# Kernel optimization log

Hardware: AMD Instinct MI355X
Metric: run time of the kernel (lower is better)

The kernel has to match this reference:

```python
import jax, jax.numpy as jnp
import numpy as np

NU, NN, NS = 50000, 20000, 2000
D_IN, D_HID, D_OUT = 128, 128, 64
LRELU_SLOPE = 0.01  # torch F.leaky_relu default


def _edges(k, n_src, n_dst, e):
    k1, k2 = jax.random.split(k)
    return (jax.random.randint(k1, (e,), 0, n_src, dtype=jnp.int32),
            jax.random.randint(k2, (e,), 0, n_dst, dtype=jnp.int32))


def setup_inputs() -> dict:
    key = jax.random.key(0)
    ks = jax.random.split(key, 32)
    fs, fd = _edges(ks[0], NU, NU, 500000)
    ps, pd = _edges(ks[1], NU, NN, 300000)
    pbs, pbd = _edges(ks[2], NN, NU, 300000)
    us, ud = _edges(ks[3], NS, NN, 150000)
    ubs, ubd = _edges(ks[4], NN, NS, 150000)
    s = 0.05
    inp = {
        "x_user": jax.random.normal(ks[5], (NU, D_IN), jnp.float32),
        "x_news": jax.random.normal(ks[6], (NN, D_IN), jnp.float32),
        "x_source": jax.random.normal(ks[7], (NS, D_IN), jnp.float32),
        # stacked per-relation GraphConv params, order:
        # [follows, posts, posted_by, publishes, published_by]
        "W1": jax.random.normal(ks[8], (5, D_IN, D_HID), jnp.float32) * s,
        "b1": jnp.zeros((5, D_HID), jnp.float32),
        "W2": jax.random.normal(ks[9], (5, D_HID, D_HID), jnp.float32) * s,
        "b2": jnp.zeros((5, D_HID), jnp.float32),
        "Wu": jax.random.normal(ks[10], (D_HID, D_OUT), jnp.float32) * s,
        "bu": jnp.zeros((D_OUT,), jnp.float32),
        "Wn": jax.random.normal(ks[11], (D_HID, D_OUT), jnp.float32) * s,
        "bn": jnp.zeros((D_OUT,), jnp.float32),
        "Ws": jax.random.normal(ks[12], (D_HID, D_OUT), jnp.float32) * s,
        "bs": jnp.zeros((D_OUT,), jnp.float32),
        "follows_src": fs, "follows_dst": fd,
        "posts_src": ps, "posts_dst": pd,
        "postedby_src": pbs, "postedby_dst": pbd,
        "publishes_src": us, "publishes_dst": ud,
        "publishedby_src": ubs, "publishedby_dst": ubd,
    }
    return inp


def _gconv(x_src, src, dst, n_dst, W, b):
    """DGL GraphConv, norm='both': D_dst^-1/2 A D_src^-1/2 X W + b."""
    n_src = x_src.shape[0]
    ones = jnp.ones(src.shape[0], x_src.dtype)
    dout = jnp.clip(jax.ops.segment_sum(ones, src, num_segments=n_src), 1.0)
    din = jnp.clip(jax.ops.segment_sum(ones, dst, num_segments=n_dst), 1.0)
    h = (x_src * jax.lax.rsqrt(dout)[:, None]) @ W  # transform before gather
    agg = jax.ops.segment_sum(h[src], dst, num_segments=n_dst)
    return agg * jax.lax.rsqrt(din)[:, None] + b


def _hetero_layer(xu, xn, xs, E, W, b):
    # mean aggregation across relations sharing a dst type
    hu = 0.5 * (_gconv(xu, E["fs"], E["fd"], NU, W[0], b[0])
                + _gconv(xn, E["pbs"], E["pbd"], NU, W[2], b[2]))
    hn = 0.5 * (_gconv(xu, E["ps"], E["pd"], NN, W[1], b[1])
                + _gconv(xs, E["us"], E["ud"], NN, W[3], b[3]))
    hs = _gconv(xn, E["ubs"], E["ubd"], NS, W[4], b[4])
    return hu, hn, hs


def reference(x_user, x_news, x_source, W1, b1, W2, b2, Wu, bu, Wn, bn, Ws, bs,
              follows_src, follows_dst, posts_src, posts_dst,
              postedby_src, postedby_dst, publishes_src, publishes_dst,
              publishedby_src, publishedby_dst):
    E = {"fs": follows_src, "fd": follows_dst, "ps": posts_src, "pd": posts_dst,
         "pbs": postedby_src, "pbd": postedby_dst, "us": publishes_src,
         "ud": publishes_dst, "ubs": publishedby_src, "ubd": publishedby_dst}
    lrelu = lambda v: jax.nn.leaky_relu(v, LRELU_SLOPE)
    hu, hn, hs = _hetero_layer(x_user, x_news, x_source, E, W1, b1)
    hu, hn, hs = lrelu(hu), lrelu(hn), lrelu(hs)
    hu, hn, hs = _hetero_layer(hu, hn, hs, E, W2, b2)
    hu, hn, hs = lrelu(hu), lrelu(hn), lrelu(hs)
    ou = hu @ Wu + bu
    on = hn @ Wn + bn
    os_ = hs @ Ws + bs
    return (ou, on, os_, hu, hn, hs)
```

## Files before the change

kernel.cpp:

```cpp
#include <hip/hip_runtime.h>

#define LRELU 0.01f

static const int kNU = 50000, kNN = 20000, kNS = 2000;
static const int DOUT_OFF[5] = {0, 100000, 170000, 240000, 262000};
static const int DIN_OFF[5]  = {50000, 150000, 190000, 242000, 282000};
static const int RP_OFF[5]   = {0, 50001, 70002, 120003, 140004};
static const int CSR_OFF[5]  = {0, 500000, 800000, 1100000, 1250000};

using bf16x8 = __attribute__((ext_vector_type(8))) short;
using u16x8  = __attribute__((ext_vector_type(8))) unsigned short;
using f32x4  = __attribute__((ext_vector_type(4))) float;

__device__ __forceinline__ float bf2f(unsigned short u) {
  return __uint_as_float(((unsigned)u) << 16);
}
__device__ __forceinline__ unsigned short f2bf(float f) {
  unsigned u = __float_as_uint(f);
  u += 0x7FFFu + ((u >> 16) & 1u);
  return (unsigned short)(u >> 16);
}


struct TJob { const float* X; const float* W; unsigned short* Y; int M; };
struct PrepJob { const float* W0; const float* W128; unsigned short* hi;
                 unsigned short* lo; int NOUT; int lgK; int bstart; };
struct AArgs { const int* esrc[5]; const int* edst[5]; int* pos; int* partial;
               TJob tj[5]; PrepJob pj[6]; };

__device__ __forceinline__ void transform_body(const TJob& p, int bxl, int t) {
  int w = t >> 6, l = t & 63;
  int lo16 = l & 15, hi4 = l >> 4;
  int m0 = bxl * 64;
  int M = p.M;
  f32x4 acc[4][2] = {};
  for (int s = 0; s < 4; ++s) {
    int kbase = s * 32 + hi4 * 8;
    bf16x8 af[4];
#pragma unroll
    for (int mf = 0; mf < 4; ++mf) {
      int row = m0 + mf * 16 + lo16;
      row = row < M ? row : M - 1;
      const float* xr = &p.X[(size_t)row * 128 + kbase];
      float4 xa = *(const float4*)xr;
      float4 xb = *(const float4*)(xr + 4);
      af[mf][0] = (short)f2bf(xa.x); af[mf][1] = (short)f2bf(xa.y);
      af[mf][2] = (short)f2bf(xa.z); af[mf][3] = (short)f2bf(xa.w);
      af[mf][4] = (short)f2bf(xb.x); af[mf][5] = (short)f2bf(xb.y);
      af[mf][6] = (short)f2bf(xb.z); af[mf][7] = (short)f2bf(xb.w);
    }
#pragma unroll
    for (int nf = 0; nf < 2; ++nf) {
      int n = (w * 2 + nf) * 16 + lo16;
      bf16x8 bh, bl;
#pragma unroll
      for (int j = 0; j < 8; ++j) {
        float wv = p.W[(size_t)(kbase + j) * 128 + n];
        unsigned short h = f2bf(wv);
        bh[j] = (short)h;
        bl[j] = (short)f2bf(wv - bf2f(h));
      }
#pragma unroll
      for (int mf = 0; mf < 4; ++mf) {
        acc[mf][nf] = __builtin_amdgcn_mfma_f32_16x16x32_bf16(af[mf], bh, acc[mf][nf], 0, 0, 0);
        acc[mf][nf] = __builtin_amdgcn_mfma_f32_16x16x32_bf16(af[mf], bl, acc[mf][nf], 0, 0, 0);
      }
    }
  }
#pragma unroll
  for (int nf = 0; nf < 2; ++nf) {
    int col = (w * 2 + nf) * 16 + lo16;
#pragma unroll
    for (int mf = 0; mf < 4; ++mf) {
#pragma unroll
      for (int rr = 0; rr < 4; ++rr) {
        int row = m0 + mf * 16 + hi4 * 4 + rr;
        if (row < M) p.Y[(size_t)row * 128 + col] = f2bf(acc[mf][nf][rr]);
      }
    }
  }
}

__global__ __launch_bounds__(256) void k_histA(AArgs a) {
  __shared__ int hbin[8192];
  int bx = blockIdx.x;
  int t = threadIdx.x;
  if (bx < 336) {
    constexpr int DSTART[6] = {0, 112, 160, 272, 320, 336};
    constexpr int NDT[5] = {50000, 20000, 50000, 20000, 2000};
    constexpr int CS[5]  = {31250, 18750, 18750, 9375, 9375};
    constexpr int EE[5]  = {500000, 300000, 300000, 150000, 150000};
    constexpr int PB[5]  = {0, 800000, 1120000, 1920000, 2240000};
    constexpr int COFF[5] = {0, 500000, 800000, 1100000, 1250000};
    int r = 0;
    while (bx >= DSTART[r + 1]) ++r;
    int local = bx - DSTART[r];
    int g = local >> 4, c = local & 15;
    int nd = NDT[r];
    int gbase = g * 8192;
    int gend = gbase + 8192 < nd ? gbase + 8192 : nd;
    const int* dst = a.edst[r];
    int* pos = a.pos + COFF[r];
    int elo = c * CS[r];
    int ehi = elo + CS[r] < EE[r] ? elo + CS[r] : EE[r];
    for (int j = t; j < 8192; j += 256) hbin[j] = 0;
    __syncthreads();
    for (int e = elo + t; e < ehi; e += 256) {
      int d = dst[e];
      if (d >= gbase && d < gend) pos[e] = atomicAdd(&hbin[d - gbase], 1);
    }
    __syncthreads();
    int* out = a.partial + PB[r] + (size_t)c * nd + gbase;
    int nn = gend - gbase;
    for (int j = t; j < nn; j += 256) out[j] = hbin[j];
  } else if (bx < 672) {
    constexpr int OSTART[6] = {0, 112, 224, 272, 288, 336};
    constexpr int NST[5] = {50000, 50000, 20000, 2000, 20000};
    constexpr int CS[5]  = {31250, 18750, 18750, 9375, 9375};
    constexpr int EE[5]  = {500000, 300000, 300000, 150000, 150000};
    constexpr int PB[5]  = {2272000, 3072000, 3872000, 4192000, 4224000};
    int idx = bx - 336;
    int r = 0;
    while (idx >= OSTART[r + 1]) ++r;
    int local = idx - OSTART[r];
    int g = local >> 4, c = local & 15;
    int ns = NST[r];
    int gbase = g * 8192;
    int gend = gbase + 8192 < ns ? gbase + 8192 : ns;
    const int* src = a.esrc[r];
    int elo = c * CS[r];
    int ehi = elo + CS[r] < EE[r] ? elo + CS[r] : EE[r];
    for (int j = t; j < 8192; j += 256) hbin[j] = 0;
    __syncthreads();
    for (int e = elo + t; e < ehi; e += 256) {
      int s = src[e];
      if (s >= gbase && s < gend) atomicAdd(&hbin[s - gbase], 1);
    }
    __syncthreads();
    int* out = a.partial + PB[r] + (size_t)c * ns + gbase;
    int nn = gend - gbase;
    for (int j = t; j < nn; j += 256) out[j] = hbin[j];
  } else if (bx < 2894) {
    constexpr int TSTART[6] = {0, 782, 1564, 1877, 1909, 2222};
    int ti = bx - 672, r = 0;
    while (ti >= TSTART[r + 1]) ++r;
    transform_body(a.tj[r], ti - TSTART[r], t);
  } else {
    int b = bx - 2894, ji = 0;
    while (ji < 5 && b >= a.pj[ji + 1].bstart) ++ji;
    PrepJob p = a.pj[ji];
    int eidx = (b - p.bstart) * 256 + t;
    int K = 1 << p.lgK;
    int n = eidx >> p.lgK, k = eidx & (K - 1);
    if (n >= p.NOUT) return;
    float w = (k < 128) ? p.W0[k * p.NOUT + n] : p.W128[(k - 128) * p.NOUT + n];
    unsigned short h = f2bf(w);
    float res = w - bf2f(h);
    p.hi[n * K + k] = h;
    p.lo[n * K + k] = f2bf(res);
  }
}


struct BArgs { int* partial; int* cnt; float* rs; };

__global__ __launch_bounds__(256) void k_scanB(BArgs a) {
  int bx = blockIdx.x;
  int t = threadIdx.x;
  if (bx < 555) {
    int i = bx * 256 + t;
    if (i >= 142000) return;
    constexpr int NDT[5] = {50000, 20000, 50000, 20000, 2000};
    constexpr int PB[5]  = {0, 800000, 1120000, 1920000, 2240000};
    constexpr int DOFF[5] = {50000, 150000, 190000, 242000, 282000};
    int r, d;
    if      (i < 50000)  { r = 0; d = i; }
    else if (i < 70000)  { r = 1; d = i - 50000; }
    else if (i < 120000) { r = 2; d = i - 70000; }
    else if (i < 140000) { r = 3; d = i - 120000; }
    else                 { r = 4; d = i - 140000; }
    int nd = NDT[r];
    int* p = a.partial + PB[r] + d;
    int run = 0;
#pragma unroll
    for (int c = 0; c < 16; ++c) {
      int v = p[(size_t)c * nd];
      p[(size_t)c * nd] = run;
      run += v;
    }
    a.cnt[DOFF[r] + d] = run;
    a.rs[DOFF[r] + d] = rsqrtf((float)(run > 1 ? run : 1));
  } else {
    int i = (bx - 555) * 256 + t;
    if (i >= 142000) return;
    constexpr int NST[5] = {50000, 50000, 20000, 2000, 20000};
    constexpr int PB[5]  = {2272000, 3072000, 3872000, 4192000, 4224000};
    constexpr int OOFF[5] = {0, 100000, 170000, 240000, 262000};
    int r, s;
    if      (i < 50000)  { r = 0; s = i; }
    else if (i < 100000) { r = 1; s = i - 50000; }
    else if (i < 120000) { r = 2; s = i - 100000; }
    else if (i < 122000) { r = 3; s = i - 120000; }
    else                 { r = 4; s = i - 122000; }
    int ns = NST[r];
    const int* p = a.partial + PB[r] + s;
    int sum = 0;
#pragma unroll
    for (int c = 0; c < 16; ++c) sum += p[(size_t)c * ns];
    a.rs[OOFF[r] + s] = rsqrtf((float)(sum > 1 ? sum : 1));
  }
}


struct S3Args { const int* cnt; int* rp; };

__global__ __launch_bounds__(256) void k_scan3(S3Args a) {
  constexpr int CSTART[6] = {0, 49, 69, 118, 138, 140};
  constexpr int NDT[5] = {50000, 20000, 50000, 20000, 2000};
  constexpr int DOFF[5] = {50000, 150000, 190000, 242000, 282000};
  constexpr int RPOFF[5] = {0, 50001, 70002, 120003, 140004};
  int bx = blockIdx.x, r = 0;
  while (bx >= CSTART[r + 1]) ++r;
  int chunk = bx - CSTART[r];
  int nch = CSTART[r + 1] - CSTART[r];
  int n = NDT[r];
  const int* cnt = a.cnt + DOFF[r];
  int* rp = a.rp + RPOFF[r];
  int t = threadIdx.x;
  __shared__ int sd[256];
  __shared__ int choff_sh;
  int lim = chunk * 1024;
  int pre = 0;
  for (int j = t; j < lim; j += 256) pre += cnt[j];
  sd[t] = pre;
  __syncthreads();
  for (int off = 128; off > 0; off >>= 1) {
    if (t < off) sd[t] += sd[t + off];
    __syncthreads();
  }
  if (t == 0) choff_sh = sd[0];
  __syncthreads();
  int idx0 = lim + t * 4;
  int v[4];
#pragma unroll
  for (int j = 0; j < 4; ++j) v[j] = (idx0 + j < n) ? cnt[idx0 + j] : 0;
  int tsum = v[0] + v[1] + v[2] + v[3];
  sd[t] = tsum;
  __syncthreads();
  for (int s = 1; s < 256; s <<= 1) {
    int add = (t >= s) ? sd[t - s] : 0;
    __syncthreads();
    sd[t] += add;
    __syncthreads();
  }
  int off = choff_sh + sd[t] - tsum;
#pragma unroll
  for (int j = 0; j < 4; ++j) {
    if (idx0 + j < n) rp[idx0 + j] = off;
    off += v[j];
  }
  if (chunk == nch - 1 && t == 255) rp[n] = choff_sh + sd[255];
}


struct CArgs { const int* esrc[5]; const int* edst[5]; const int* pos;
               const int* rp; const int* partial; int* csr; };

__global__ __launch_bounds__(256) void k_buildC(CArgs a) {
  constexpr int ESTART[6] = {0, 1954, 3126, 4298, 4884, 5470};
  constexpr int NDT[5] = {50000, 20000, 50000, 20000, 2000};
  constexpr int CS[5]  = {31250, 18750, 18750, 9375, 9375};
  constexpr int EE[5]  = {500000, 300000, 300000, 150000, 150000};
  constexpr int PB[5]  = {0, 800000, 1120000, 1920000, 2240000};
  constexpr int RPOFF[5] = {0, 50001, 70002, 120003, 140004};
  constexpr int COFF[5] = {0, 500000, 800000, 1100000, 1250000};
  int bx = blockIdx.x, r = 0;
  while (bx >= ESTART[r + 1]) ++r;
  int i = (bx - ESTART[r]) * 256 + threadIdx.x;
  if (i < EE[r]) {
    int d = a.edst[r][i];
    int c = i / CS[r];
    int slot = a.rp[RPOFF[r] + d] + a.partial[PB[r] + (size_t)c * NDT[r] + d]
             + a.pos[COFF[r] + i];
    a.csr[COFF[r] + slot] = a.esrc[r][i];
  }
}


#define GROW(vv, cc)                                                              \
  _Pragma("unroll") for (int q = 0; q < 8; ++q)                                   \
      acc[q] = fmaf(__uint_as_float(((unsigned)(unsigned short)vv[q]) << 16), cc, acc[q]);

__device__ __forceinline__ void gat_accum(const int* __restrict__ rp,
    const int* __restrict__ csr, const unsigned short* __restrict__ Y,
    const float* __restrict__ rso, int wid, int sub, float* acc) {
  int e0 = rp[wid], e1 = rp[wid + 1];
  for (int base = e0; base < e1; base += 16) {
    int m = e1 - base;
    if (m > 16) m = 16;
    int ei = base + (sub < m ? sub : 0);
    int se = csr[ei];
    float sc = rso[se];
    if (m == 16) {
      bf16x8 v[16];
#pragma unroll
      for (int j = 0; j < 16; ++j) {
        int sj = __shfl(se, j, 16);
        v[j] = *(const bf16x8*)&Y[(size_t)sj * 128 + sub * 8];
      }
#pragma unroll
      for (int j = 0; j < 16; ++j) {
        float cj = __shfl(sc, j, 16);
        GROW(v[j], cj)
      }
    } else {
      int j = 0;
      for (; j + 8 <= m; j += 8) {
        int s0 = __shfl(se, j, 16), s1 = __shfl(se, j + 1, 16);
        int s2 = __shfl(se, j + 2, 16), s3 = __shfl(se, j + 3, 16);
        int s4 = __shfl(se, j + 4, 16), s5 = __shfl(se, j + 5, 16);
        int s6 = __shfl(se, j + 6, 16), s7 = __shfl(se, j + 7, 16);
        float c0 = __shfl(sc, j, 16), c1 = __shfl(sc, j + 1, 16);
        float c2 = __shfl(sc, j + 2, 16), c3 = __shfl(sc, j + 3, 16);
        float c4 = __shfl(sc, j + 4, 16), c5 = __shfl(sc, j + 5, 16);
        float c6 = __shfl(sc, j + 6, 16), c7 = __shfl(sc, j + 7, 16);
        bf16x8 v0 = *(const bf16x8*)&Y[(size_t)s0 * 128 + sub * 8];
        bf16x8 v1 = *(const bf16x8*)&Y[(size_t)s1 * 128 + sub * 8];
        bf16x8 v2 = *(const bf16x8*)&Y[(size_t)s2 * 128 + sub * 8];
        bf16x8 v3 = *(const bf16x8*)&Y[(size_t)s3 * 128 + sub * 8];
        bf16x8 v4 = *(const bf16x8*)&Y[(size_t)s4 * 128 + sub * 8];
        bf16x8 v5 = *(const bf16x8*)&Y[(size_t)s5 * 128 + sub * 8];
        bf16x8 v6 = *(const bf16x8*)&Y[(size_t)s6 * 128 + sub * 8];
        bf16x8 v7 = *(const bf16x8*)&Y[(size_t)s7 * 128 + sub * 8];
        GROW(v0, c0) GROW(v1, c1) GROW(v2, c2) GROW(v3, c3)
        GROW(v4, c4) GROW(v5, c5) GROW(v6, c6) GROW(v7, c7)
      }
      for (; j < m; ++j) {
        int s0 = __shfl(se, j, 16);
        float c0 = __shfl(sc, j, 16);
        bf16x8 v0 = *(const bf16x8*)&Y[(size_t)s0 * 128 + sub * 8];
        GROW(v0, c0)
      }
    }
  }
}


struct G1Rel { const int* rp; const int* csr; const unsigned short* Y;
               const float* rso; const float* rsi; };
struct G1Args { G1Rel rel[5]; const float* b;
                unsigned short* hU; unsigned short* hN; unsigned short* hS; };

__global__ __launch_bounds__(256) void k_gather1(G1Args a) {
  int bx = blockIdx.x;
  int t = threadIdx.x;
  int sub = t & 15;
  float acc[8], tot[8];
#pragma unroll
  for (int q = 0; q < 8; ++q) acc[q] = 0.f;
  if (bx < 3125) {
    int wid = bx * 16 + (t >> 4);
    gat_accum(a.rel[0].rp, a.rel[0].csr, a.rel[0].Y, a.rel[0].rso, wid, sub, acc);
    float s0 = a.rel[0].rsi[wid];
#pragma unroll
    for (int q = 0; q < 8; ++q) { tot[q] = s0 * acc[q]; acc[q] = 0.f; }
    gat_accum(a.rel[2].rp, a.rel[2].csr, a.rel[2].Y, a.rel[2].rso, wid, sub, acc);
    float s2 = a.rel[2].rsi[wid];
    const float* b0 = a.b;
    const float* b2 = a.b + 2 * 128;
    u16x8 o;
#pragma unroll
    for (int q = 0; q < 8; ++q) {
      float v = 0.5f * (tot[q] + s2 * acc[q] + b0[sub * 8 + q] + b2[sub * 8 + q]);
      v = v >= 0.f ? v : LRELU * v;
      o[q] = f2bf(v);
    }
    *(u16x8*)&a.hU[(size_t)wid * 128 + sub * 8] = o;
  } else if (bx < 4375) {
    int wid = (bx - 3125) * 16 + (t >> 4);
    gat_accum(a.rel[1].rp, a.rel[1].csr, a.rel[1].Y, a.rel[1].rso, wid, sub, acc);
    float s1 = a.rel[1].rsi[wid];
#pragma unroll
    for (int q = 0; q < 8; ++q) { tot[q] = s1 * acc[q]; acc[q] = 0.f; }
    gat_accum(a.rel[3].rp, a.rel[3].csr, a.rel[3].Y, a.rel[3].rso, wid, sub, acc);
    float s3 = a.rel[3].rsi[wid];
    const float* b1v = a.b + 128;
    const float* b3 = a.b + 3 * 128;
    u16x8 o;
#pragma unroll
    for (int q = 0; q < 8; ++q) {
      float v = 0.5f * (tot[q] + s3 * acc[q] + b1v[sub * 8 + q] + b3[sub * 8 + q]);
      v = v >= 0.f ? v : LRELU * v;
      o[q] = f2bf(v);
    }
    *(u16x8*)&a.hN[(size_t)wid * 128 + sub * 8] = o;
  } else {
    int wid = (bx - 4375) * 16 + (t >> 4);
    gat_accum(a.rel[4].rp, a.rel[4].csr, a.rel[4].Y, a.rel[4].rso, wid, sub, acc);
    float s4 = a.rel[4].rsi[wid];
    const float* b4 = a.b + 4 * 128;
    u16x8 o;
#pragma unroll
    for (int q = 0; q < 8; ++q) {
      float v = s4 * acc[q] + b4[sub * 8 + q];
      v = v >= 0.f ? v : LRELU * v;
      o[q] = f2bf(v);
    }
    *(u16x8*)&a.hS[(size_t)wid * 128 + sub * 8] = o;
  }
}


struct RelG {
  const int* rp; const int* csr; const unsigned short* xb;
  const float* rso; const float* rsi;
  unsigned short* out; int stride; int ooff; int nd;
};
struct GArgs { RelG rel[5]; };

__global__ __launch_bounds__(256) void k_gather(GArgs a) {
  constexpr int GSTART[6] = {0, 3125, 4375, 7500, 8750, 8875};
  int bx = blockIdx.x, r = 0;
  while (bx >= GSTART[r + 1]) ++r;
  RelG g = a.rel[r];
  int t = threadIdx.x;
  int sub = t & 15;
  int wid = (bx - GSTART[r]) * 16 + (t >> 4);
  if (wid >= g.nd) return;
  float acc[8];
#pragma unroll
  for (int q = 0; q < 8; ++q) acc[q] = 0.f;
  gat_accum(g.rp, g.csr, g.xb, g.rso, wid, sub, acc);
  float si = g.rsi[wid];
  u16x8 o;
#pragma unroll
  for (int q = 0; q < 8; ++q) o[q] = f2bf(acc[q] * si);
  *(u16x8*)&g.out[(size_t)wid * g.stride + g.ooff + sub * 8] = o;
}


struct MJob { const unsigned short* A; const unsigned short* Wh; const unsigned short* Wl;
              const float* b0; const float* b1; float scale; int lrelu;
              float* H; int ldh; unsigned short* Hb; int M; int bstart; };
struct MArgs { MJob j[3]; };

template <int KCH, int NW>
__device__ __forceinline__ void mgemm_body(const MJob& p, int bxl) {
  constexpr int KP = KCH * 128;
  int t = threadIdx.x;
  int w = t >> 6, l = t & 63;
  int lo16 = l & 15, hi4 = l >> 4;
  int m0 = bxl * 64;
  int M = p.M;
  const unsigned short* A = p.A;
  f32x4 acc[4][NW] = {};
  for (int s = 0; s < KP / 32; ++s) {
    int kbase = s * 32 + hi4 * 8;
    bf16x8 af[4];
#pragma unroll
    for (int mf = 0; mf < 4; ++mf) {
      int row = m0 + mf * 16 + lo16;
      row = row < M ? row : M - 1;
      af[mf] = *(const bf16x8*)&A[(size_t)row * KP + kbase];
    }
#pragma unroll
    for (int nf = 0; nf < NW; ++nf) {
      int n = (w * NW + nf) * 16 + lo16;
      bf16x8 bh = *(const bf16x8*)&p.Wh[(size_t)n * KP + kbase];
      bf16x8 bl = *(const bf16x8*)&p.Wl[(size_t)n * KP + kbase];
#pragma unroll
      for (int mf = 0; mf < 4; ++mf) {
        acc[mf][nf] = __builtin_amdgcn_mfma_f32_16x16x32_bf16(af[mf], bh, acc[mf][nf], 0, 0, 0);
        acc[mf][nf] = __builtin_amdgcn_mfma_f32_16x16x32_bf16(af[mf], bl, acc[mf][nf], 0, 0, 0);
      }
    }
  }
#pragma unroll
  for (int nf = 0; nf < NW; ++nf) {
    int col = (w * NW + nf) * 16 + lo16;
    float bs = p.b0[col];
    if (p.b1) bs += p.b1[col];
#pragma unroll
    for (int mf = 0; mf < 4; ++mf) {
#pragma unroll
      for (int rr = 0; rr < 4; ++rr) {
        int row = m0 + mf * 16 + hi4 * 4 + rr;
        if (row < M) {
          float o = p.scale * (acc[mf][nf][rr] + bs);
          if (p.lrelu) o = o >= 0.f ? o : LRELU * o;
          if (p.H) p.H[(size_t)row * p.ldh + col] = o;
          if (p.Hb) p.Hb[(size_t)row * p.ldh + col] = f2bf(o);
        }
      }
    }
  }
}

__global__ __launch_bounds__(256) void k_mgemm3(MArgs a) {
  int bx = blockIdx.x;
  if (bx < a.j[1].bstart)      mgemm_body<2, 2>(a.j[0], bx);
  else if (bx < a.j[2].bstart) mgemm_body<2, 2>(a.j[1], bx - a.j[1].bstart);
  else                         mgemm_body<1, 2>(a.j[2], bx - a.j[2].bstart);
}

__global__ __launch_bounds__(256) void k_proj3(MArgs a) {
  int bx = blockIdx.x;
  if (bx < a.j[1].bstart)      mgemm_body<1, 1>(a.j[0], bx);
  else if (bx < a.j[2].bstart) mgemm_body<1, 1>(a.j[1], bx - a.j[1].bstart);
  else                         mgemm_body<1, 1>(a.j[2], bx - a.j[2].bstart);
}


extern "C" void kernel_launch(void* const* d_in, const int* in_sizes, int n_in,
                              void* d_out, int out_size, void* d_ws, size_t ws_size,
                              hipStream_t stream) {
  const float* xu = (const float*)d_in[0];
  const float* xn = (const float*)d_in[1];
  const float* xs = (const float*)d_in[2];
  const float* W1 = (const float*)d_in[3];
  const float* b1 = (const float*)d_in[4];
  const float* W2 = (const float*)d_in[5];
  const float* b2 = (const float*)d_in[6];
  const float* Wu = (const float*)d_in[7];
  const float* bu = (const float*)d_in[8];
  const float* Wn = (const float*)d_in[9];
  const float* bn = (const float*)d_in[10];
  const float* Wsrc = (const float*)d_in[11];
  const float* bsrc = (const float*)d_in[12];
  const int* SRC[5] = {(const int*)d_in[13], (const int*)d_in[15], (const int*)d_in[17],
                       (const int*)d_in[19], (const int*)d_in[21]};
  const int* DST[5] = {(const int*)d_in[14], (const int*)d_in[16], (const int*)d_in[18],
                       (const int*)d_in[20], (const int*)d_in[22]};

  int* ws_i = (int*)d_ws;
  int* rp = ws_i;
  int* csr = ws_i + 142008;
  int* pos = ws_i + 1542008;
  int* cnt = ws_i + 2942328;
  float* rs = (float*)(ws_i + 3226328);
  unsigned short* wt = (unsigned short*)(rs + 284000);
  unsigned short* aggU = wt + 376832;
  unsigned short* aggN = aggU + 12800000;
  unsigned short* aggS = aggN + 5120000;
  unsigned short* xbU = aggS + 256000;
  unsigned short* xbN = xbU + 6400000;
  unsigned short* xbS = xbN + 2560000;

  unsigned short* L2U_h = wt + 163840, * L2U_l = wt + 196608;
  unsigned short* L2N_h = wt + 229376, * L2N_l = wt + 262144;
  unsigned short* L2S_h = wt + 294912, * L2S_l = wt + 311296;
  unsigned short* PU_h = wt + 327680, * PU_l = wt + 335872;
  unsigned short* PN_h = wt + 344064, * PN_l = wt + 352256;
  unsigned short* PS_h = wt + 360448, * PS_l = wt + 368640;

  float* outf = (float*)d_out;
  float* ou = outf;
  float* on = outf + 3200000;
  float* osrc = outf + 4480000;
  float* hu = outf + 4608000;
  float* hn = outf + 11008000;
  float* hs = outf + 13568000;

  int* partial = (int*)outf;

  unsigned short* Yb = (unsigned short*)(outf + 4608000);
  unsigned short* Y0 = Yb;
  unsigned short* Y1 = Y0 + 6400000;
  unsigned short* Y2 = Y1 + 6400000;
  unsigned short* Y3 = Y2 + 2560000;
  unsigned short* Y4 = Y3 + 256000;

  AArgs aa;
  for (int r = 0; r < 5; ++r) { aa.esrc[r] = SRC[r]; aa.edst[r] = DST[r]; }
  aa.pos = pos;
  aa.partial = partial;
  aa.tj[0] = {xu, W1 + 0 * 16384, Y0, kNU};
  aa.tj[1] = {xu, W1 + 1 * 16384, Y1, kNU};
  aa.tj[2] = {xn, W1 + 2 * 16384, Y2, kNN};
  aa.tj[3] = {xs, W1 + 3 * 16384, Y3, kNS};
  aa.tj[4] = {xn, W1 + 4 * 16384, Y4, kNN};
  aa.pj[0] = {W2, W2 + 2 * 16384, L2U_h, L2U_l, 128, 8, 0};
  aa.pj[1] = {W2 + 16384, W2 + 3 * 16384, L2N_h, L2N_l, 128, 8, 128};
  aa.pj[2] = {W2 + 4 * 16384, nullptr, L2S_h, L2S_l, 128, 7, 256};
  aa.pj[3] = {Wu, nullptr, PU_h, PU_l, 64, 7, 320};
  aa.pj[4] = {Wn, nullptr, PN_h, PN_l, 64, 7, 352};
  aa.pj[5] = {Wsrc, nullptr, PS_h, PS_l, 64, 7, 384};
  k_histA<<<3310, 256, 0, stream>>>(aa);

  BArgs ba = {partial, cnt, rs};
  k_scanB<<<1110, 256, 0, stream>>>(ba);

  S3Args s3 = {cnt, rp};
  k_scan3<<<140, 256, 0, stream>>>(s3);

  CArgs ca;
  for (int r = 0; r < 5; ++r) { ca.esrc[r] = SRC[r]; ca.edst[r] = DST[r]; }
  ca.pos = pos;
  ca.rp = rp;
  ca.partial = partial;
  ca.csr = csr;
  k_buildC<<<5470, 256, 0, stream>>>(ca);

  G1Args g1;
  const unsigned short* YT[5] = {Y0, Y1, Y2, Y3, Y4};
  for (int r = 0; r < 5; ++r)
    g1.rel[r] = {rp + RP_OFF[r], csr + CSR_OFF[r], YT[r],
                 rs + DOUT_OFF[r], rs + DIN_OFF[r]};
  g1.b = b1;
  g1.hU = xbU; g1.hN = xbN; g1.hS = xbS;
  k_gather1<<<4500, 256, 0, stream>>>(g1);

  {
    const unsigned short* XIN[5] = {xbU, xbU, xbN, xbS, xbN};
    unsigned short* OUT[5] = {aggU, aggN, aggU, aggN, aggS};
    const int OSTR[5] = {256, 256, 256, 256, 128};
    const int OOFF[5] = {0, 0, 128, 128, 0};
    GArgs ga;
    for (int r = 0; r < 5; ++r)
      ga.rel[r] = {rp + RP_OFF[r], csr + CSR_OFF[r], XIN[r], rs + DOUT_OFF[r],
                   rs + DIN_OFF[r], OUT[r], OSTR[r], OOFF[r],
                   (r == 0 || r == 2) ? kNU : (r == 4 ? kNS : kNN)};
    k_gather<<<8875, 256, 0, stream>>>(ga);
    MArgs ma;
    ma.j[0] = {aggU, L2U_h, L2U_l, b2, b2 + 2 * 128, 0.5f, 1, hu, 128, xbU, kNU, 0};
    ma.j[1] = {aggN, L2N_h, L2N_l, b2 + 128, b2 + 3 * 128, 0.5f, 1, hn, 128, xbN, kNN, 782};
    ma.j[2] = {aggS, L2S_h, L2S_l, b2 + 4 * 128, nullptr, 1.0f, 1, hs, 128, xbS, kNS, 1095};
    k_mgemm3<<<1127, 256, 0, stream>>>(ma);
  }

  MArgs pm;
  pm.j[0] = {xbU, PU_h, PU_l, bu, nullptr, 1.0f, 0, ou, 64, nullptr, kNU, 0};
  pm.j[1] = {xbN, PN_h, PN_l, bn, nullptr, 1.0f, 0, on, 64, nullptr, kNN, 782};
  pm.j[2] = {xbS, PS_h, PS_l, bsrc, nullptr, 1.0f, 0, osrc, 64, nullptr, kNS, 1095};
  k_proj3<<<1127, 256, 0, stream>>>(pm);
}
```

Measured before the change: 330.5 us.

## Transform-before-gather for layer 2 and pack histogram bins as 16-bit pairs

Layer 2 used to gather first and then run a concatenated-K GEMM. It now applies the per-relation weight transform first (k_trans5) and then gathers through a fused kernel that does the combine, bias, leaky-relu and both fp32 and bf16 stores, matching how layer 1 is done. This swaps the wide 256-col aggregate buffers for per-relation transformed features, so the larger gather now reads 128-col bf16 rows of transformed features per edge and the GEMM shrinks to K=128. The histogram kernel also packs two 16-bit counters per shared int, so each block covers 16384 bins and fewer blocks are launched. This relies on no bin count exceeding 65535 per chunk and on the in-place writes to xb buffers being ordered safely.

```diff
diff --git a/kernel.cpp b/kernel.cpp
--- a/kernel.cpp
+++ b/kernel.cpp
@@ -23,10 +23,10 @@
 
 
 struct TJob { const float* X; const float* W; unsigned short* Y; int M; };
-struct PrepJob { const float* W0; const float* W128; unsigned short* hi;
-                 unsigned short* lo; int NOUT; int lgK; int bstart; };
+struct PrepJob { const float* W0; unsigned short* hi; unsigned short* lo;
+                 int NOUT; int bstart; };
 struct AArgs { const int* esrc[5]; const int* edst[5]; int* pos; int* partial;
-               TJob tj[5]; PrepJob pj[6]; };
+               TJob tj[5]; PrepJob pj[8]; };
 
 __device__ __forceinline__ void transform_body(const TJob& p, int bxl, int t) {
   int w = t >> 6, l = t & 63;
@@ -82,11 +82,11 @@
 }
 
 __global__ __launch_bounds__(256) void k_histA(AArgs a) {
-  __shared__ int hbin[8192];
+  __shared__ unsigned hbin[8192];
   int bx = blockIdx.x;
   int t = threadIdx.x;
-  if (bx < 336) {
-    constexpr int DSTART[6] = {0, 112, 160, 272, 320, 336};
+  if (bx < 208) {
+    constexpr int DSTART[6] = {0, 64, 96, 160, 192, 208};
     constexpr int NDT[5] = {50000, 20000, 50000, 20000, 2000};
     constexpr int CS[5]  = {31250, 18750, 18750, 9375, 9375};
     constexpr int EE[5]  = {500000, 300000, 300000, 150000, 150000};
@@ -97,8 +97,8 @@
     int local = bx - DSTART[r];
     int g = local >> 4, c = local & 15;
     int nd = NDT[r];
-    int gbase = g * 8192;
-    int gend = gbase + 8192 < nd ? gbase + 8192 : nd;
+    int gbase = g * 16384;
+    int gend = gbase + 16384 < nd ? gbase + 16384 : nd;
     const int* dst = a.edst[r];
     int* pos = a.pos + COFF[r];
     int elo = c * CS[r];
@@ -107,26 +107,32 @@
     __syncthreads();
     for (int e = elo + t; e < ehi; e += 256) {
       int d = dst[e];
-      if (d >= gbase && d < gend) pos[e] = atomicAdd(&hbin[d - gbase], 1);
+      if (d >= gbase && d < gend) {
+        int bin = d - gbase;
+        int sh = (bin & 1) * 16;
+        unsigned old = atomicAdd(&hbin[bin >> 1], 1u << sh);
+        pos[e] = (int)((old >> sh) & 0xffffu);
+      }
     }
     __syncthreads();
     int* out = a.partial + PB[r] + (size_t)c * nd + gbase;
     int nn = gend - gbase;
-    for (int j = t; j < nn; j += 256) out[j] = hbin[j];
-  } else if (bx < 672) {
-    constexpr int OSTART[6] = {0, 112, 224, 272, 288, 336};
+    for (int j = t; j < nn; j += 256)
+      out[j] = (int)((hbin[j >> 1] >> ((j & 1) * 16)) & 0xffffu);
+  } else if (bx < 416) {
+    constexpr int OSTART[6] = {0, 64, 128, 160, 176, 208};
     constexpr int NST[5] = {50000, 50000, 20000, 2000, 20000};
     constexpr int CS[5]  = {31250, 18750, 18750, 9375, 9375};
     constexpr int EE[5]  = {500000, 300000, 300000, 150000, 150000};
     constexpr int PB[5]  = {2272000, 3072000, 3872000, 4192000, 4224000};
-    int idx = bx - 336;
+    int idx = bx - 208;
     int r = 0;
     while (idx >= OSTART[r + 1]) ++r;
     int local = idx - OSTART[r];
     int g = local >> 4, c = local & 15;
     int ns = NST[r];
-    int gbase = g * 8192;
-    int gend = gbase + 8192 < ns ? gbase + 8192 : ns;
+    int gbase = g * 16384;
+    int gend = gbase + 16384 < ns ? gbase + 16384 : ns;
     const int* src = a.esrc[r];
     int elo = c * CS[r];
     int ehi = elo + CS[r] < EE[r] ? elo + CS[r] : EE[r];
@@ -134,30 +140,31 @@
     __syncthreads();
     for (int e = elo + t; e < ehi; e += 256) {
       int s = src[e];
-      if (s >= gbase && s < gend) atomicAdd(&hbin[s - gbase], 1);
+      if (s >= gbase && s < gend)
+        atomicAdd(&hbin[(s - gbase) >> 1], 1u << (((s - gbase) & 1) * 16));
     }
     __syncthreads();
     int* out = a.partial + PB[r] + (size_t)c * ns + gbase;
     int nn = gend - gbase;
-    for (int j = t; j < nn; j += 256) out[j] = hbin[j];
-  } else if (bx < 2894) {
+    for (int j = t; j < nn; j += 256)
+      out[j] = (int)((hbin[j >> 1] >> ((j & 1) * 16)) & 0xffffu);
+  } else if (bx < 2638) {
     constexpr int TSTART[6] = {0, 782, 1564, 1877, 1909, 2222};
-    int ti = bx - 672, r = 0;
+    int ti = bx - 416, r = 0;
     while (ti >= TSTART[r + 1]) ++r;
     transform_body(a.tj[r], ti - TSTART[r], t);
   } else {
-    int b = bx - 2894, ji = 0;
-    while (ji < 5 && b >= a.pj[ji + 1].bstart) ++ji;
+    int b = bx - 2638, ji = 0;
+    while (ji < 7 && b >= a.pj[ji + 1].bstart) ++ji;
     PrepJob p = a.pj[ji];
     int eidx = (b - p.bstart) * 256 + t;
-    int K = 1 << p.lgK;
-    int n = eidx >> p.lgK, k = eidx & (K - 1);
+    int n = eidx >> 7, k = eidx & 127;
     if (n >= p.NOUT) return;
-    float w = (k < 128) ? p.W0[k * p.NOUT + n] : p.W128[(k - 128) * p.NOUT + n];
+    float w = p.W0[k * p.NOUT + n];
     unsigned short h = f2bf(w);
     float res = w - bf2f(h);
-    p.hi[n * K + k] = h;
-    p.lo[n * K + k] = f2bf(res);
+    p.hi[n * 128 + k] = h;
+    p.lo[n * 128 + k] = f2bf(res);
   }
 }
 
@@ -411,38 +418,9 @@
 }
 
 
-struct RelG {
-  const int* rp; const int* csr; const unsigned short* xb;
-  const float* rso; const float* rsi;
-  unsigned short* out; int stride; int ooff; int nd;
-};
-struct GArgs { RelG rel[5]; };
-
-__global__ __launch_bounds__(256) void k_gather(GArgs a) {
-  constexpr int GSTART[6] = {0, 3125, 4375, 7500, 8750, 8875};
-  int bx = blockIdx.x, r = 0;
-  while (bx >= GSTART[r + 1]) ++r;
-  RelG g = a.rel[r];
-  int t = threadIdx.x;
-  int sub = t & 15;
-  int wid = (bx - GSTART[r]) * 16 + (t >> 4);
-  if (wid >= g.nd) return;
-  float acc[8];
-#pragma unroll
-  for (int q = 0; q < 8; ++q) acc[q] = 0.f;
-  gat_accum(g.rp, g.csr, g.xb, g.rso, wid, sub, acc);
-  float si = g.rsi[wid];
-  u16x8 o;
-#pragma unroll
-  for (int q = 0; q < 8; ++q) o[q] = f2bf(acc[q] * si);
-  *(u16x8*)&g.out[(size_t)wid * g.stride + g.ooff + sub * 8] = o;
-}
-
-
 struct MJob { const unsigned short* A; const unsigned short* Wh; const unsigned short* Wl;
               const float* b0; const float* b1; float scale; int lrelu;
               float* H; int ldh; unsigned short* Hb; int M; int bstart; };
-struct MArgs { MJob j[3]; };
 
 template <int KCH, int NW>
 __device__ __forceinline__ void mgemm_body(const MJob& p, int bxl) {
@@ -478,7 +456,7 @@
 #pragma unroll
   for (int nf = 0; nf < NW; ++nf) {
     int col = (w * NW + nf) * 16 + lo16;
-    float bs = p.b0[col];
+    float bs = p.b0 ? p.b0[col] : 0.f;
     if (p.b1) bs += p.b1[col];
 #pragma unroll
     for (int mf = 0; mf < 4; ++mf) {
@@ -496,18 +474,90 @@
   }
 }
 
-__global__ __launch_bounds__(256) void k_mgemm3(MArgs a) {
+struct M5Args { MJob j[5]; };
+__global__ __launch_bounds__(256) void k_trans5(M5Args a) {
   int bx = blockIdx.x;
-  if (bx < a.j[1].bstart)      mgemm_body<2, 2>(a.j[0], bx);
-  else if (bx < a.j[2].bstart) mgemm_body<2, 2>(a.j[1], bx - a.j[1].bstart);
-  else                         mgemm_body<1, 2>(a.j[2], bx - a.j[2].bstart);
-}
-
+  int ji = 0;
+  while (ji < 4 && bx >= a.j[ji + 1].bstart) ++ji;
+  mgemm_body<1, 2>(a.j[ji], bx - a.j[ji].bstart);
+}
+
+struct MArgs { MJob j[3]; };
 __global__ __launch_bounds__(256) void k_proj3(MArgs a) {
   int bx = blockIdx.x;
   if (bx < a.j[1].bstart)      mgemm_body<1, 1>(a.j[0], bx);
   else if (bx < a.j[2].bstart) mgemm_body<1, 1>(a.j[1], bx - a.j[1].bstart);
   else                         mgemm_body<1, 1>(a.j[2], bx - a.j[2].bstart);
+}
+
+
+struct G2Args { G1Rel rel[5]; const float* b;
+                float* HU; float* HN; float* HS;
+                unsigned short* hU; unsigned short* hN; unsigned short* hS; };
+
+__device__ __forceinline__ void g2_store(float* H, unsigned short* Hb,
+                                         int wid, int sub, const float* v) {
+  float4 f0 = {v[0], v[1], v[2], v[3]};
+  float4 f1 = {v[4], v[5], v[6], v[7]};
+  *(float4*)&H[(size_t)wid * 128 + sub * 8] = f0;
+  *(float4*)&H[(size_t)wid * 128 + sub * 8 + 4] = f1;
+  u16x8 o;
+#pragma unroll
+  for (int q = 0; q < 8; ++q) o[q] = f2bf(v[q]);
+  *(u16x8*)&Hb[(size_t)wid * 128 + sub * 8] = o;
+}
+
+__global__ __launch_bounds__(256) void k_gather2(G2Args a) {
+  int bx = blockIdx.x;
+  int t = threadIdx.x;
+  int sub = t & 15;
+  float acc[8], tot[8], v[8];
+#pragma unroll
+  for (int q = 0; q < 8; ++q) acc[q] = 0.f;
+  if (bx < 3125) {
+    int wid = bx * 16 + (t >> 4);
+    gat_accum(a.rel[0].rp, a.rel[0].csr, a.rel[0].Y, a.rel[0].rso, wid, sub, acc);
+    float s0 = a.rel[0].rsi[wid];
+#pragma unroll
+    for (int q = 0; q < 8; ++q) { tot[q] = s0 * acc[q]; acc[q] = 0.f; }
+    gat_accum(a.rel[2].rp, a.rel[2].csr, a.rel[2].Y, a.rel[2].rso, wid, sub, acc);
+    float s2 = a.rel[2].rsi[wid];
+    const float* b0 = a.b;
+    const float* b2 = a.b + 2 * 128;
+#pragma unroll
+    for (int q = 0; q < 8; ++q) {
+      float x = 0.5f * (tot[q] + s2 * acc[q] + b0[sub * 8 + q] + b2[sub * 8 + q]);
+      v[q] = x >= 0.f ? x : LRELU * x;
+    }
+    g2_store(a.HU, a.hU, wid, sub, v);
+  } else if (bx < 4375) {
+    int wid = (bx - 3125) * 16 + (t >> 4);
+    gat_accum(a.rel[1].rp, a.rel[1].csr, a.rel[1].Y, a.rel[1].rso, wid, sub, acc);
+    float s1 = a.rel[1].rsi[wid];
+#pragma unroll
+    for (int q = 0; q < 8; ++q) { tot[q] = s1 * acc[q]; acc[q] = 0.f; }
+    gat_accum(a.rel[3].rp, a.rel[3].csr, a.rel[3].Y, a.rel[3].rso, wid, sub, acc);
+    float s3 = a.rel[3].rsi[wid];
+    const float* b1v = a.b + 128;
+    const float* b3 = a.b + 3 * 128;
+#pragma unroll
+    for (int q = 0; q < 8; ++q) {
+      float x = 0.5f * (tot[q] + s3 * acc[q] + b1v[sub * 8 + q] + b3[sub * 8 + q]);
+      v[q] = x >= 0.f ? x : LRELU * x;
+    }
+    g2_store(a.HN, a.hN, wid, sub, v);
+  } else {
+    int wid = (bx - 4375) * 16 + (t >> 4);
+    gat_accum(a.rel[4].rp, a.rel[4].csr, a.rel[4].Y, a.rel[4].rso, wid, sub, acc);
+    float s4 = a.rel[4].rsi[wid];
+    const float* b4 = a.b + 4 * 128;
+#pragma unroll
+    for (int q = 0; q < 8; ++q) {
+      float x = s4 * acc[q] + b4[sub * 8 + q];
+      v[q] = x >= 0.f ? x : LRELU * x;
+    }
+    g2_store(a.HS, a.hS, wid, sub, v);
+  }
 }
 
 
@@ -539,19 +589,22 @@
   int* cnt = ws_i + 2942328;
   float* rs = (float*)(ws_i + 3226328);
   unsigned short* wt = (unsigned short*)(rs + 284000);
-  unsigned short* aggU = wt + 376832;
-  unsigned short* aggN = aggU + 12800000;
-  unsigned short* aggS = aggN + 5120000;
-  unsigned short* xbU = aggS + 256000;
+  unsigned short* Y2region = wt + 376832;
+  unsigned short* xbU = Y2region + 18176000;
   unsigned short* xbN = xbU + 6400000;
   unsigned short* xbS = xbN + 2560000;
 
-  unsigned short* L2U_h = wt + 163840, * L2U_l = wt + 196608;
-  unsigned short* L2N_h = wt + 229376, * L2N_l = wt + 262144;
-  unsigned short* L2S_h = wt + 294912, * L2S_l = wt + 311296;
-  unsigned short* PU_h = wt + 327680, * PU_l = wt + 335872;
-  unsigned short* PN_h = wt + 344064, * PN_l = wt + 352256;
-  unsigned short* PS_h = wt + 360448, * PS_l = wt + 368640;
+  unsigned short* Y2_0 = Y2region;
+  unsigned short* Y2_1 = Y2_0 + 6400000;
+  unsigned short* Y2_2 = Y2_1 + 6400000;
+  unsigned short* Y2_4 = Y2_2 + 2560000;
+  unsigned short* Y2_3 = Y2_4 + 2560000;
+
+  unsigned short* W2h[5], * W2l[5];
+  for (int r = 0; r < 5; ++r) { W2h[r] = wt + r * 32768; W2l[r] = wt + r * 32768 + 16384; }
+  unsigned short* PU_h = wt + 163840, * PU_l = wt + 172032;
+  unsigned short* PN_h = wt + 180224, * PN_l = wt + 188416;
+  unsigned short* PS_h = wt + 196608, * PS_l = wt + 204800;
 
   float* outf = (float*)d_out;
   float* ou = outf;
@@ -566,8 +619,8 @@
   unsigned short* Yb = (unsigned short*)(outf + 4608000);
   unsigned short* Y0 = Yb;
   unsigned short* Y1 = Y0 + 6400000;
-  unsigned short* Y2 = Y1 + 6400000;
-  unsigned short* Y3 = Y2 + 2560000;
+  unsigned short* Y2a = Y1 + 6400000;
+  unsigned short* Y3 = Y2a + 2560000;
   unsigned short* Y4 = Y3 + 256000;
 
   AArgs aa;
@@ -576,16 +629,15 @@
   aa.partial = partial;
   aa.tj[0] = {xu, W1 + 0 * 16384, Y0, kNU};
   aa.tj[1] = {xu, W1 + 1 * 16384, Y1, kNU};
-  aa.tj[2] = {xn, W1 + 2 * 16384, Y2, kNN};
+  aa.tj[2] = {xn, W1 + 2 * 16384, Y2a, kNN};
   aa.tj[3] = {xs, W1 + 3 * 16384, Y3, kNS};
   aa.tj[4] = {xn, W1 + 4 * 16384, Y4, kNN};
-  aa.pj[0] = {W2, W2 + 2 * 16384, L2U_h, L2U_l, 128, 8, 0};
-  aa.pj[1] = {W2 + 16384, W2 + 3 * 16384, L2N_h, L2N_l, 128, 8, 128};
-  aa.pj[2] = {W2 + 4 * 16384, nullptr, L2S_h, L2S_l, 128, 7, 256};
-  aa.pj[3] = {Wu, nullptr, PU_h, PU_l, 64, 7, 320};
-  aa.pj[4] = {Wn, nullptr, PN_h, PN_l, 64, 7, 352};
-  aa.pj[5] = {Wsrc, nullptr, PS_h, PS_l, 64, 7, 384};
-  k_histA<<<3310, 256, 0, stream>>>(aa);
+  for (int r = 0; r < 5; ++r)
+    aa.pj[r] = {W2 + r * 16384, W2h[r], W2l[r], 128, r * 64};
+  aa.pj[5] = {Wu, PU_h, PU_l, 64, 320};
+  aa.pj[6] = {Wn, PN_h, PN_l, 64, 352};
+  aa.pj[7] = {Wsrc, PS_h, PS_l, 64, 384};
+  k_histA<<<3054, 256, 0, stream>>>(aa);
 
   BArgs ba = {partial, cnt, rs};
   k_scanB<<<1110, 256, 0, stream>>>(ba);
@@ -602,7 +654,7 @@
   k_buildC<<<5470, 256, 0, stream>>>(ca);
 
   G1Args g1;
-  const unsigned short* YT[5] = {Y0, Y1, Y2, Y3, Y4};
+  const unsigned short* YT[5] = {Y0, Y1, Y2a, Y3, Y4};
   for (int r = 0; r < 5; ++r)
     g1.rel[r] = {rp + RP_OFF[r], csr + CSR_OFF[r], YT[r],
                  rs + DOUT_OFF[r], rs + DIN_OFF[r]};
@@ -610,23 +662,23 @@
   g1.hU = xbU; g1.hN = xbN; g1.hS = xbS;
   k_gather1<<<4500, 256, 0, stream>>>(g1);
 
-  {
-    const unsigned short* XIN[5] = {xbU, xbU, xbN, xbS, xbN};
-    unsigned short* OUT[5] = {aggU, aggN, aggU, aggN, aggS};
-    const int OSTR[5] = {256, 256, 256, 256, 128};
-    const int OOFF[5] = {0, 0, 128, 128, 0};
-    GArgs ga;
-    for (int r = 0; r < 5; ++r)
-      ga.rel[r] = {rp + RP_OFF[r], csr + CSR_OFF[r], XIN[r], rs + DOUT_OFF[r],
-                   rs + DIN_OFF[r], OUT[r], OSTR[r], OOFF[r],
-                   (r == 0 || r == 2) ? kNU : (r == 4 ? kNS : kNN)};
-    k_gather<<<8875, 256, 0, stream>>>(ga);
-    MArgs ma;
-    ma.j[0] = {aggU, L2U_h, L2U_l, b2, b2 + 2 * 128, 0.5f, 1, hu, 128, xbU, kNU, 0};
-    ma.j[1] = {aggN, L2N_h, L2N_l, b2 + 128, b2 + 3 * 128, 0.5f, 1, hn, 128, xbN, kNN, 782};
-    ma.j[2] = {aggS, L2S_h, L2S_l, b2 + 4 * 128, nullptr, 1.0f, 1, hs, 128, xbS, kNS, 1095};
-    k_mgemm3<<<1127, 256, 0, stream>>>(ma);
-  }
+  M5Args t5;
+  t5.j[0] = {xbU, W2h[0], W2l[0], nullptr, nullptr, 1.0f, 0, nullptr, 128, Y2_0, kNU, 0};
+  t5.j[1] = {xbU, W2h[1], W2l[1], nullptr, nullptr, 1.0f, 0, nullptr, 128, Y2_1, kNU, 782};
+  t5.j[2] = {xbN, W2h[2], W2l[2], nullptr, nullptr, 1.0f, 0, nullptr, 128, Y2_2, kNN, 1564};
+  t5.j[3] = {xbS, W2h[3], W2l[3], nullptr, nullptr, 1.0f, 0, nullptr, 128, Y2_3, kNS, 1877};
+  t5.j[4] = {xbN, W2h[4], W2l[4], nullptr, nullptr, 1.0f, 0, nullptr, 128, Y2_4, kNN, 1909};
+  k_trans5<<<2222, 256, 0, stream>>>(t5);
+
+  G2Args g2;
+  const unsigned short* Y2T[5] = {Y2_0, Y2_1, Y2_2, Y2_3, Y2_4};
+  for (int r = 0; r < 5; ++r)
+    g2.rel[r] = {rp + RP_OFF[r], csr + CSR_OFF[r], Y2T[r],
+                 rs + DOUT_OFF[r], rs + DIN_OFF[r]};
+  g2.b = b2;
+  g2.HU = hu; g2.HN = hn; g2.HS = hs;
+  g2.hU = xbU; g2.hN = xbN; g2.hS = xbS;
+  k_gather2<<<4500, 256, 0, stream>>>(g2);
 
   MArgs pm;
   pm.j[0] = {xbU, PU_h, PU_l, bu, nullptr, 1.0f, 0, ou, 64, nullptr, kNU, 0};
```

Measured after the change: 343.8 us. +4.0%, slower.
